# Kernel tuning notes

Hardware: AMD Instinct MI355X
Metric: run time of the kernel (lower is better)

Reference implementation:

```python
import jax, jax.numpy as jnp
import numpy as np

H = 32      # num_attention_heads
HD = 64     # head_dim
MD = 64     # qk_mqa_dim (rope dim)
EPS = 1e-6
SCALING = (HD + MD) ** -0.5
NEG = -1e9


def rms_norm(x, w):
    var = jnp.mean(jnp.square(x), axis=-1, keepdims=True)
    return x * jax.lax.rsqrt(var + EPS) * w


def rotate_half(x):
    x1, x2 = jnp.split(x, 2, axis=-1)
    return jnp.concatenate([-x2, x1], axis=-1)


def apply_rope(x, cos, sin):
    return x * cos + rotate_half(x) * sin


def setup_inputs() -> dict:
    key = jax.random.key(0)
    ks = jax.random.split(key, 6)
    B, S, D = 1, 2048, 2048
    QR, KVR = 1024, 896
    hidden_states = jax.random.normal(ks[0], (B, S, D), jnp.float32)
    # real rotary tables for the MD-dim rope subspace
    inv_freq = 1.0 / (10000.0 ** (np.arange(0, MD, 2, dtype=np.float32) / MD))
    freqs = np.arange(S, dtype=np.float32)[:, None] * inv_freq[None, :]
    emb = np.concatenate([freqs, freqs], axis=-1)  # [S, MD]
    cos = jnp.asarray(np.cos(emb), jnp.float32)
    sin = jnp.asarray(np.sin(emb), jnp.float32)
    s = 0.02
    Wqa = jax.random.normal(ks[1], (QR, D), jnp.float32) * s
    q_ln_w = jnp.ones((QR,), jnp.float32)
    Wqb = jax.random.normal(ks[2], (H * (HD + MD), QR), jnp.float32) * s
    Wkva = jax.random.normal(ks[3], (KVR + MD, D), jnp.float32) * s
    kv_ln_w = jnp.ones((KVR,), jnp.float32)
    Wkvb = jax.random.normal(ks[4], (2 * H * HD, KVR), jnp.float32) * s
    Wo = jax.random.normal(ks[5], (D, H * HD), jnp.float32) * s
    return {"hidden_states": hidden_states, "cos": cos, "sin": sin,
            "Wqa": Wqa, "q_ln_w": q_ln_w, "Wqb": Wqb,
            "Wkva": Wkva, "kv_ln_w": kv_ln_w, "Wkvb": Wkvb, "Wo": Wo}


def reference(hidden_states, cos, sin, Wqa, q_ln_w, Wqb, Wkva, kv_ln_w, Wkvb, Wo):
    B, S, D = hidden_states.shape
    KVR = kv_ln_w.shape[0]
    # Q: LoRA down -> RMSNorm -> up (weights pre-absorbed with rope split)
    q = rms_norm(hidden_states @ Wqa.T, q_ln_w) @ Wqb.T      # [B,S,H*(HD+MD)]
    q = q.reshape(B, S, H, HD + MD).transpose(0, 2, 1, 3)     # [B,H,S,HD+MD]
    q_nope, q_rope = q[..., :HD], q[..., HD:]
    # KV: shared compressed latent + MQA rope key
    ckv = hidden_states @ Wkva.T                               # [B,S,KVR+MD]
    kv_nope, k_rope = ckv[..., :KVR], ckv[..., KVR:]
    kv_nope = rms_norm(kv_nope, kv_ln_w)
    q_rope = apply_rope(q_rope, cos[None, None], sin[None, None])
    k_rope = apply_rope(k_rope[:, None], cos[None, None], sin[None, None])  # [B,1,S,MD]
    # up-project latent to per-head K_nope and V (interleaved per head)
    kv = (kv_nope @ Wkvb.T).reshape(B, S, H, 2 * HD).transpose(0, 2, 1, 3)  # [B,H,S,2*HD]
    k_nope, value = kv[..., :HD], kv[..., HD:]
    key_states = jnp.concatenate(
        [k_nope, jnp.broadcast_to(k_rope, (B, H, S, MD))], axis=-1)  # repeat_kv of rope part
    query_states = jnp.concatenate([q_nope, q_rope], axis=-1)        # [B,H,S,HD+MD]
    # causal SDPA with scaling = (head_dim + qk_mqa_dim)^-0.5
    scores = jnp.einsum('bhqd,bhkd->bhqk', query_states, key_states) * SCALING
    causal = jnp.tril(jnp.ones((S, S), bool))
    scores = jnp.where(causal[None, None], scores, NEG)
    probs = jax.nn.softmax(scores, axis=-1)
    out = jnp.einsum('bhqk,bhkd->bhqd', probs, value)                # [B,H,S,HD]
    out = out.transpose(0, 2, 1, 3).reshape(B, S, H * HD)
    return out @ Wo.T
```

## Files before the change

kernel.cpp:

```cpp
#include <hip/hip_runtime.h>
#include <stdint.h>

typedef unsigned short u16;
typedef __attribute__((ext_vector_type(4))) float f32x4;
typedef __attribute__((ext_vector_type(4))) unsigned short u16x4;
typedef __attribute__((ext_vector_type(8))) unsigned short u16x8;
typedef __attribute__((ext_vector_type(8))) short s16x8;
typedef __attribute__((ext_vector_type(4))) short s16x4;
typedef __attribute__((ext_vector_type(2))) unsigned int u32x2;

#define DEVI static __device__ __forceinline__

#define VMCNT(n) asm volatile("s_waitcnt vmcnt(" #n ")" ::: "memory")
#define SBAR() __builtin_amdgcn_s_barrier()
#define SCHED0() __builtin_amdgcn_sched_barrier(0)

DEVI u16 f2b(float f) {
  union { float f; unsigned u; } v; v.f = f;
  unsigned r = v.u + 0x7fffu + ((v.u >> 16) & 1u);
  return (u16)(r >> 16);
}
DEVI float b2f(u16 b) {
  union { unsigned u; float f; } v; v.u = ((unsigned)b) << 16;
  return v.f;
}

DEVI void gload_lds16(const void* gptr, void* lptr) {
  typedef const __attribute__((address_space(1))) unsigned gq;
  typedef __attribute__((address_space(3))) unsigned lq;
  __builtin_amdgcn_global_load_lds((gq*)(uintptr_t)gptr,
                                   (lq*)(uint32_t)(uintptr_t)lptr, 16, 0, 0);
}

DEVI unsigned cvtpk(float a, float b) {
  unsigned d;
  asm("v_cvt_pk_bf16_f32 %0, %1, %2" : "=v"(d) : "v"(a), "v"(b));
  return d;
}
DEVI f32x4 mfma16(s16x4 a, s16x4 b, f32x4 c) {
  f32x4 d;
  asm("v_mfma_f32_16x16x16_bf16 %0, %1, %2, %3" : "=v"(d) : "v"(a), "v"(b), "v"(c));
  return d;
}
DEVI float exp2a(float x) {
  float d;
  asm("v_exp_f32 %0, %1" : "=v"(d) : "v"(x));
  return d;
}

__global__ __launch_bounds__(256) void cvt_all(
    const float* __restrict__ X, const float* __restrict__ Wqa,
    const float* __restrict__ Wkva, const float* __restrict__ Wqb,
    const float* __restrict__ Wkvb, const float* __restrict__ Wo,
    u16* __restrict__ Xb, u16* __restrict__ W1, u16* __restrict__ Wqbb,
    u16* __restrict__ Wkvbb, u16* __restrict__ Wob) {
  int i = blockIdx.x * 256 + threadIdx.x;
  const int stride = gridDim.x * 256;
  for (; i < 5079040; i += stride) {
    const float* s; u16* d; int j;
    if (i < 1572864) {
      if (i < 1048576) { s = X; d = Xb; j = i; }
      else             { s = Wqa; d = W1; j = i - 1048576; }
    } else if (i < 3112960) {
      if (i < 2064384) { s = Wkva; d = W1 + 1024 * 2048; j = i - 1572864; }
      else             { s = Wqb; d = Wqbb; j = i - 2064384; }
    } else {
      if (i < 4030464) { s = Wkvb; d = Wkvbb; j = i - 3112960; }
      else             { s = Wo; d = Wob; j = i - 4030464; }
    }
    f32x4 v = *(const f32x4*)(s + (size_t)j * 4);
    u16x4 o;
    o[0] = f2b(v[0]); o[1] = f2b(v[1]); o[2] = f2b(v[2]); o[3] = f2b(v[3]);
    *(u16x4*)(d + (size_t)j * 4) = o;
  }
}

#define GEMM_STAGE(AP, BP, KK, k0, buf)                                        \
  {                                                                            \
    _Pragma("unroll") for (int p = 0; p < 4; ++p) {                            \
      const int c = tid + p * 256;                                             \
      const int row = c >> 3, j = c & 7;                                       \
      gload_lds16(AP + (size_t)(m0 + row) * (KK) + (k0) + ((j ^ (row & 7)) * 8), \
                  &As[buf][c * 8]);                                            \
    }                                                                          \
    _Pragma("unroll") for (int p = 0; p < 4; ++p) {                            \
      const int c = tid + p * 256;                                             \
      const int row = c >> 3, j = c & 7;                                       \
      gload_lds16(BP + (size_t)(n0 + row) * (KK) + (k0) + ((j ^ (row & 7)) * 8), \
                  &Bs[buf][c * 8]);                                            \
    }                                                                          \
  }

#define GEMM_COMPUTE(cur)                                                      \
  _Pragma("unroll") for (int kk = 0; kk < 64; kk += 32) {                      \
    s16x8 af[4], bfr[4];                                                       \
    _Pragma("unroll") for (int i = 0; i < 4; ++i) {                            \
      const int rA = wm * 64 + i * 16 + c15;                                   \
      af[i] = *(const s16x8*)((const char*)&As[cur][0] + rA * 128 +            \
                              (((kk + g * 8) * 2) ^ ((rA & 7) << 4)));         \
    }                                                                          \
    _Pragma("unroll") for (int i = 0; i < 4; ++i) {                            \
      const int rB = wn * 64 + i * 16 + c15;                                   \
      bfr[i] = *(const s16x8*)((const char*)&Bs[cur][0] + rB * 128 +           \
                               (((kk + g * 8) * 2) ^ ((rB & 7) << 4)));        \
    }                                                                          \
    _Pragma("unroll") for (int i = 0; i < 4; ++i)                              \
      _Pragma("unroll") for (int j = 0; j < 4; ++j)                            \
        acc[i][j] = __builtin_amdgcn_mfma_f32_16x16x32_bf16(af[i], bfr[j],     \
                                                            acc[i][j], 0, 0, 0); \
  }

#define GEMM_PROLOG                                                            \
  const int tid = threadIdx.x;                                                 \
  const int lane = tid & 63, w = tid >> 6;                                     \
  const int wm = w >> 1, wn = w & 1;                                           \
  const int c15 = lane & 15, g = lane >> 4;                                    \
  const int m0 = blockIdx.y * 128, n0 = blockIdx.x * 128;                      \
  f32x4 acc[4][4] = {};

#define GEMM_LOOP(AP, BP, KK)                                                  \
  GEMM_STAGE(AP, BP, KK, 0, 0);                                                \
  const int nk = (KK) >> 6;                                                    \
  for (int kt = 0; kt < nk; ++kt) {                                            \
    const int cur = kt & 1;                                                    \
    if (kt + 1 < nk) {                                                         \
      GEMM_STAGE(AP, BP, KK, (kt + 1) << 6, cur ^ 1);                          \
      VMCNT(8);                                                                \
    } else {                                                                   \
      VMCNT(0);                                                                \
    }                                                                          \
    SBAR(); SCHED0();                                                          \
    GEMM_COMPUTE(cur);                                                         \
    SBAR(); SCHED0();                                                          \
  }

#define GEMM_LOOP3(AP, BP, KK)                                                 \
  GEMM_STAGE(AP, BP, KK, 0, 0);                                                \
  GEMM_STAGE(AP, BP, KK, 64, 1);                                               \
  const int nk = (KK) >> 6;                                                    \
  int bufc = 0;                                                                \
  for (int kt = 0; kt < nk; ++kt) {                                            \
    const int nxt = (bufc + 2 >= 3) ? bufc - 1 : bufc + 2;                     \
    if (kt + 2 < nk) {                                                         \
      GEMM_STAGE(AP, BP, KK, (kt + 2) << 6, nxt);                              \
      VMCNT(16);                                                               \
    } else if (kt + 1 < nk) {                                                  \
      VMCNT(8);                                                                \
    } else {                                                                   \
      VMCNT(0);                                                                \
    }                                                                          \
    SBAR(); SCHED0();                                                          \
    GEMM_COMPUTE(bufc);                                                        \
    SBAR(); SCHED0();                                                          \
    bufc = (bufc + 1 == 3) ? 0 : bufc + 1;                                     \
  }

template <int OUT_BF16>
__global__ __launch_bounds__(256) void gemm_out(const u16* __restrict__ A,
                                                const u16* __restrict__ B,
                                                void* __restrict__ Cv,
                                                int M, int N, int K) {
  __shared__ __align__(16) u16 As[3][128 * 64];
  __shared__ __align__(16) u16 Bs[3][128 * 64];
  GEMM_PROLOG
  GEMM_LOOP3(A, B, K)
#pragma unroll
  for (int i = 0; i < 4; ++i)
#pragma unroll
    for (int j = 0; j < 4; ++j) {
      const int mr = m0 + wm * 64 + i * 16 + g * 4;
      const int nc = n0 + wn * 64 + j * 16 + c15;
#pragma unroll
      for (int r = 0; r < 4; ++r) {
        if (OUT_BF16)
          ((u16*)Cv)[(size_t)(mr + r) * N + nc] = f2b(acc[i][j][r]);
        else
          ((float*)Cv)[(size_t)(mr + r) * N + nc] = acc[i][j][r];
      }
    }
}

__global__ __launch_bounds__(256) void gemm2_fused(
    const u16* __restrict__ qn, const u16* __restrict__ Wqbb,
    const u16* __restrict__ kvn, const u16* __restrict__ Wkvbb,
    u16* __restrict__ qraw, char* __restrict__ KbB, char* __restrict__ VtB) {
  __shared__ __align__(16) u16 As[2][128 * 64];
  __shared__ __align__(16) u16 Bs[2][128 * 64];
  const int z = blockIdx.z;
  const u16* A = z ? kvn : qn;
  const u16* B = z ? Wkvbb : Wqbb;
  const int K = z ? 896 : 1024;
  GEMM_PROLOG
  GEMM_LOOP(A, B, K)

  if (z == 0) {
#pragma unroll
    for (int i = 0; i < 4; ++i)
#pragma unroll
      for (int j = 0; j < 4; ++j) {
        const int mr = m0 + wm * 64 + i * 16 + g * 4;
        const int nc = n0 + wn * 64 + j * 16 + c15;
#pragma unroll
        for (int r = 0; r < 4; ++r)
          qraw[(size_t)(mr + r) * 4096 + nc] = f2b(acc[i][j][r]);
      }
  } else {
    const int h = n0 >> 7;
#pragma unroll
    for (int i = 0; i < 4; ++i)
#pragma unroll
      for (int j = 0; j < 4; ++j) {
        const int mr = m0 + wm * 64 + i * 16 + g * 4;
        if (wn == 0) {
          const int d = j * 16 + c15;
#pragma unroll
          for (int r = 0; r < 4; ++r) {
            const int s = mr + r;
            *(u16*)(KbB + ((size_t)(h * 2048 + s) << 8) +
                    ((2 * d) ^ ((s & 7) << 4))) = f2b(acc[i][j][r]);
          }
        } else {
          const int d = j * 16 + c15;
          u16x4 o;
#pragma unroll
          for (int r = 0; r < 4; ++r) o[r] = f2b(acc[i][j][r]);
          *(u16x4*)(VtB + ((size_t)(h * 64 + d) << 12) +
                    ((2 * mr) ^ ((d & 7) << 4))) = o;
        }
      }
  }
}

DEVI float block_sum(float v, float* sbuf, int tid) {
#pragma unroll
  for (int o = 32; o; o >>= 1) v += __shfl_xor(v, o, 64);
  __syncthreads();
  if ((tid & 63) == 0) sbuf[tid >> 6] = v;
  __syncthreads();
  return sbuf[0] + sbuf[1] + sbuf[2] + sbuf[3];
}

__global__ __launch_bounds__(256) void norm_rope(const u16* __restrict__ C1b,
    const float* __restrict__ qw, const float* __restrict__ kw,
    const float* __restrict__ cosb, const float* __restrict__ sinb,
    u16* __restrict__ qn, u16* __restrict__ kvn, char* __restrict__ KbB) {
  __shared__ float sbuf[4];
  __shared__ __align__(16) u16 rv[64];
  const int s = blockIdx.x, tid = threadIdx.x;
  const u16* row = C1b + (size_t)s * 2048;

  u16x4 qv4 = *(const u16x4*)(row + tid * 4);
  float q0 = b2f(qv4[0]), q1 = b2f(qv4[1]), q2 = b2f(qv4[2]), q3 = b2f(qv4[3]);
  float ss = q0*q0 + q1*q1 + q2*q2 + q3*q3;
  ss = block_sum(ss, sbuf, tid);
  const float scale = rsqrtf(ss * (1.f / 1024.f) + 1e-6f);
  {
    f32x4 wv = *(const f32x4*)(qw + tid * 4);
    u16x4 o;
    o[0] = f2b(q0 * scale * wv[0]); o[1] = f2b(q1 * scale * wv[1]);
    o[2] = f2b(q2 * scale * wv[2]); o[3] = f2b(q3 * scale * wv[3]);
    *(u16x4*)(qn + (size_t)s * 1024 + tid * 4) = o;
  }

  float ss2 = 0.f;
  float k0 = 0, k1 = 0, k2 = 0, k3 = 0;
  if (tid < 224) {
    u16x4 kv4 = *(const u16x4*)(row + 1024 + tid * 4);
    k0 = b2f(kv4[0]); k1 = b2f(kv4[1]); k2 = b2f(kv4[2]); k3 = b2f(kv4[3]);
    ss2 = k0*k0 + k1*k1 + k2*k2 + k3*k3;
  }
  ss2 = block_sum(ss2, sbuf, tid);
  const float sc2 = rsqrtf(ss2 * (1.f / 896.f) + 1e-6f);
  if (tid < 224) {
    f32x4 wv = *(const f32x4*)(kw + tid * 4);
    u16x4 o;
    o[0] = f2b(k0 * sc2 * wv[0]); o[1] = f2b(k1 * sc2 * wv[1]);
    o[2] = f2b(k2 * sc2 * wv[2]); o[3] = f2b(k3 * sc2 * wv[3]);
    *(u16x4*)(kvn + (size_t)s * 896 + tid * 4) = o;
  }

  if (tid < 64) {
    const int d = tid;
    const float x = b2f(row[1920 + d]);
    const float part = b2f(row[1920 + (d < 32 ? d + 32 : d - 32)]);
    const float cv = cosb[s * 64 + d], sv = sinb[s * 64 + d];
    rv[d] = f2b(d < 32 ? (x * cv - part * sv) : (x * cv + part * sv));
  }
  __syncthreads();
  {
    const int h = tid >> 3, c8 = tid & 7;
    const u16x8 v = *(const u16x8*)&rv[c8 * 8];
    *(u16x8*)(KbB + ((size_t)(h * 2048 + s) << 8) +
              ((128 + c8 * 16) ^ ((s & 7) << 4))) = v;
  }
}

__global__ __launch_bounds__(256) void attn_fwd(
    const u16* __restrict__ Qb, const u16* __restrict__ Kb,
    const u16* __restrict__ Vt, const float* __restrict__ cosb,
    const float* __restrict__ sinb, u16* __restrict__ attn) {
  __shared__ __align__(16) u16 Klds[2][64 * 128];
  __shared__ __align__(16) u16 Vlds[2][64 * 64];
  const int tid = threadIdx.x;
  const int lane = tid & 63, w = tid >> 6;
  const int c15 = lane & 15, g = lane >> 4;
  const int orig = blockIdx.x;
  const int xcd = orig & 7, l = orig >> 3;
  const int h = xcd * 4 + (l & 3);
  const int x = l >> 2;
  const int qb = (x < 8) ? (15 - x) : (x - 8);
  const int wmin = qb * 128 + w * 32;
  const int wmax = wmin + 31;
  const char* KbHB = (const char*)Kb + ((size_t)h << 19);
  const char* VtHB = (const char*)Vt + ((size_t)h << 18);
  const float SC2 = 0.12753860478587782f;

  s16x8 qf[2][4];
#pragma unroll
  for (int qa = 0; qa < 2; ++qa) {
    const int qrow = wmin + qa * 16 + c15;
    const u16* qp = Qb + (size_t)qrow * 4096 + h * 128;
    u16x8 x0 = *(const u16x8*)(qp + g * 8);
    u16x8 x1 = *(const u16x8*)(qp + 32 + g * 8);
    u16x8 x2 = *(const u16x8*)(qp + 64 + g * 8);
    u16x8 x3 = *(const u16x8*)(qp + 96 + g * 8);
    const float* cb = cosb + (size_t)qrow * 64 + g * 8;
    const float* sb = sinb + (size_t)qrow * 64 + g * 8;
#pragma unroll
    for (int i = 0; i < 8; ++i) {
      qf[qa][0][i] = (short)f2b(b2f(x0[i]) * SC2);
      qf[qa][1][i] = (short)f2b(b2f(x1[i]) * SC2);
      const float f2 = b2f(x2[i]), f3 = b2f(x3[i]);
      qf[qa][2][i] = (short)f2b((f2 * cb[i] - f3 * sb[i]) * SC2);
      qf[qa][3][i] = (short)f2b((f3 * cb[32 + i] + f2 * sb[32 + i]) * SC2);
    }
  }

  const int nt = 2 * qb + 2;
  auto STAGE = [&](int t, int buf) {
    const int kv0 = t << 6;
#pragma unroll
    for (int p = 0; p < 4; ++p) {
      const int c = tid + p * 256;
      gload_lds16(KbHB + ((size_t)(kv0 + (c >> 4)) << 8) + (c & 15) * 16,
                  (char*)Klds[buf] + c * 16);
    }
#pragma unroll
    for (int p = 0; p < 2; ++p) {
      const int c = tid + p * 256;
      gload_lds16(VtHB + ((size_t)(c >> 3) << 12) + 2 * kv0 + (c & 7) * 16,
                  (char*)Vlds[buf] + c * 16);
    }
  };

  f32x4 acc[2][4] = {};
  float m[2] = {-1e9f, -1e9f}, ssum[2] = {0.f, 0.f};

  STAGE(0, 0);

  for (int t = 0; t < nt; ++t) {
    const int cur = t & 1;
    const int kv0 = t << 6;
    if (t + 1 < nt) {
      STAGE(t + 1, cur ^ 1);
      VMCNT(6);
    } else {
      VMCNT(0);
    }
    SBAR();
    SCHED0();

    if (kv0 <= wmax) {
      const u16* Kc = Klds[cur];
      const u16* Vc = Vlds[cur];

      float pv[2][4][4];
      __builtin_amdgcn_s_setprio(1);
#pragma unroll
      for (int kvh = 0; kvh < 4; ++kvh) {
        s16x8 kf[4];
        const int rb = (kvh * 16 + c15) * 256;
#pragma unroll
        for (int d0 = 0; d0 < 4; ++d0)
          kf[d0] = *(const s16x8*)((const char*)Kc + rb +
                                   ((d0 * 64 + g * 16) ^ ((c15 & 7) << 4)));
#pragma unroll
        for (int qa = 0; qa < 2; ++qa) {
          f32x4 s4 = {};
#pragma unroll
          for (int d0 = 0; d0 < 4; ++d0)
            s4 = __builtin_amdgcn_mfma_f32_16x16x32_bf16(kf[d0], qf[qa][d0], s4, 0, 0, 0);
          pv[qa][kvh][0] = s4[0]; pv[qa][kvh][1] = s4[1];
          pv[qa][kvh][2] = s4[2]; pv[qa][kvh][3] = s4[3];
        }
      }
      __builtin_amdgcn_s_setprio(0);

      if (kv0 + 63 > wmin) {
#pragma unroll
        for (int qa = 0; qa < 2; ++qa) {
          const int qrow = wmin + qa * 16 + c15;
#pragma unroll
          for (int kvh = 0; kvh < 4; ++kvh)
#pragma unroll
            for (int r = 0; r < 4; ++r) {
              const int kv = kv0 + kvh * 16 + g * 4 + r;
              if (kv > qrow) pv[qa][kvh][r] = -1e9f;
            }
        }
      }

      s16x4 pB[2][4];
#pragma unroll
      for (int qa = 0; qa < 2; ++qa) {
        float pm = -1e9f;
#pragma unroll
        for (int kvh = 0; kvh < 4; ++kvh)
#pragma unroll
          for (int r = 0; r < 4; ++r) pm = fmaxf(pm, pv[qa][kvh][r]);
        pm = fmaxf(pm, __shfl_xor(pm, 16, 64));
        pm = fmaxf(pm, __shfl_xor(pm, 32, 64));
        if (!__all(pm - m[qa] <= 8.f)) {
          const float mnew = fmaxf(m[qa], pm);
          const float alpha = exp2a(m[qa] - mnew);
          ssum[qa] *= alpha;
#pragma unroll
          for (int dt = 0; dt < 4; ++dt) acc[qa][dt] *= alpha;
          m[qa] = mnew;
        }
#pragma unroll
        for (int kvh = 0; kvh < 4; ++kvh)
#pragma unroll
          for (int r = 0; r < 4; ++r) {
            const float p = exp2a(pv[qa][kvh][r] - m[qa]);
            pv[qa][kvh][r] = p;
            ssum[qa] += p;
          }
#pragma unroll
        for (int ks = 0; ks < 4; ++ks) {
          u32x2 pw;
          pw[0] = cvtpk(pv[qa][ks][0], pv[qa][ks][1]);
          pw[1] = cvtpk(pv[qa][ks][2], pv[qa][ks][3]);
          pB[qa][ks] = __builtin_bit_cast(s16x4, pw);
        }
      }

      __builtin_amdgcn_s_setprio(1);
#pragma unroll
      for (int dt = 0; dt < 4; ++dt) {
        const int rb2 = (dt * 16 + c15) * 128;
#pragma unroll
        for (int ks = 0; ks < 4; ++ks) {
          s16x4 vf = *(const s16x4*)((const char*)Vc + rb2 +
                                     ((ks * 32 + g * 8) ^ ((c15 & 7) << 4)));
          acc[0][dt] = mfma16(vf, pB[0][ks], acc[0][dt]);
          acc[1][dt] = mfma16(vf, pB[1][ks], acc[1][dt]);
        }
      }
      __builtin_amdgcn_s_setprio(0);
    }
    SBAR();
    SCHED0();
  }

#pragma unroll
  for (int qa = 0; qa < 2; ++qa) {
    float sv = ssum[qa];
    sv += __shfl_xor(sv, 16, 64);
    sv += __shfl_xor(sv, 32, 64);
    const float inv = 1.f / sv;
    const int qrow = wmin + qa * 16 + c15;
#pragma unroll
    for (int dt = 0; dt < 4; ++dt) {
      u16x4 o;
#pragma unroll
      for (int r = 0; r < 4; ++r) o[r] = f2b(acc[qa][dt][r] * inv);
      *(u16x4*)(attn + (size_t)qrow * 2048 + h * 64 + dt * 16 + g * 4) = o;
    }
  }
}

extern "C" void kernel_launch(void* const* d_in, const int* in_sizes, int n_in,
                              void* d_out, int out_size, void* d_ws, size_t ws_size,
                              hipStream_t stream) {
  const float* X    = (const float*)d_in[0];
  const float* cosb = (const float*)d_in[1];
  const float* sinb = (const float*)d_in[2];
  const float* Wqa  = (const float*)d_in[3];
  const float* qlnw = (const float*)d_in[4];
  const float* Wqb  = (const float*)d_in[5];
  const float* Wkva = (const float*)d_in[6];
  const float* klnw = (const float*)d_in[7];
  const float* Wkvb = (const float*)d_in[8];
  const float* Wo   = (const float*)d_in[9];
  float* out = (float*)d_out;
  char* ws = (char*)d_ws;

  u16*   Xb     = (u16*)(ws + 0);
  u16*   W1     = (u16*)(ws + 8388608);
  u16*   C1b    = (u16*)(ws + 16777216);
  u16*   qn     = (u16*)(ws + 33554432);
  u16*   kvn    = (u16*)(ws + 37748736);
  u16*   Wqbb   = (u16*)(ws + 41943040);
  u16*   Wkvbb  = (u16*)(ws + 50331648);
  u16*   qraw_b = (u16*)(ws + 0);
  u16*   Kb     = (u16*)(ws + 58720256);
  u16*   VtG    = (u16*)(ws + 75497472);
  u16*   attnb  = (u16*)(ws + 83886080);
  u16*   Wob    = (u16*)(ws + 92274688);

  cvt_all<<<2048, 256, 0, stream>>>(X, Wqa, Wkva, Wqb, Wkvb, Wo,
                                    Xb, W1, Wqbb, Wkvbb, Wob);

  gemm_out<1><<<dim3(16, 16), 256, 0, stream>>>(Xb, W1, C1b, 2048, 2048, 2048);

  norm_rope<<<2048, 256, 0, stream>>>(C1b, qlnw, klnw, cosb, sinb, qn, kvn, (char*)Kb);

  gemm2_fused<<<dim3(32, 16, 2), 256, 0, stream>>>(qn, Wqbb, kvn, Wkvbb,
                                                   qraw_b, (char*)Kb, (char*)VtG);

  attn_fwd<<<512, 256, 0, stream>>>(qraw_b, Kb, VtG, cosb, sinb, attnb);

  gemm_out<0><<<dim3(16, 16), 256, 0, stream>>>(attnb, Wob, out, 2048, 2048, 2048);
}
```

Measured before the change: 172.8 us.

## Load V fragments directly from global memory instead of staging through LDS

The attention kernel stops staging V tiles into shared memory. Each wave now reads its V MFMA fragments straight from global memory into registers, using an unswizzled Vt layout written by the producer kernel. The vmcnt wait count is adjusted to match the removed LDS loads. Separately, the cross-lane max reduction in the online softmax is now performed only when a rescale is needed. The aim is to cut LDS traffic and footprint, in exchange for extra global or L2 loads issued by every wave and more register pressure.

```diff
diff --git a/kernel.cpp b/kernel.cpp
--- a/kernel.cpp
+++ b/kernel.cpp
@@ -224,8 +224,7 @@
           u16x4 o;
 #pragma unroll
           for (int r = 0; r < 4; ++r) o[r] = f2b(acc[i][j][r]);
-          *(u16x4*)(VtB + ((size_t)(h * 64 + d) << 12) +
-                    ((2 * mr) ^ ((d & 7) << 4))) = o;
+          *(u16x4*)(VtB + ((size_t)(h * 64 + d) << 12) + 2 * mr) = o;
         }
       }
   }
@@ -298,9 +297,8 @@
 __global__ __launch_bounds__(256) void attn_fwd(
     const u16* __restrict__ Qb, const u16* __restrict__ Kb,
     const u16* __restrict__ Vt, const float* __restrict__ cosb,
-    const float* __restrict__ sinb, u16* __restrict__ attn) {
+    const float* __restrict__ sinb, u16* __restrict__ attnb) {
   __shared__ __align__(16) u16 Klds[2][64 * 128];
-  __shared__ __align__(16) u16 Vlds[2][64 * 64];
   const int tid = threadIdx.x;
   const int lane = tid & 63, w = tid >> 6;
   const int c15 = lane & 15, g = lane >> 4;
@@ -345,12 +343,6 @@
       gload_lds16(KbHB + ((size_t)(kv0 + (c >> 4)) << 8) + (c & 15) * 16,
                   (char*)Klds[buf] + c * 16);
     }
-#pragma unroll
-    for (int p = 0; p < 2; ++p) {
-      const int c = tid + p * 256;
-      gload_lds16(VtHB + ((size_t)(c >> 3) << 12) + 2 * kv0 + (c & 7) * 16,
-                  (char*)Vlds[buf] + c * 16);
-    }
   };
 
   f32x4 acc[2][4] = {};
@@ -363,7 +355,7 @@
     const int kv0 = t << 6;
     if (t + 1 < nt) {
       STAGE(t + 1, cur ^ 1);
-      VMCNT(6);
+      VMCNT(4);
     } else {
       VMCNT(0);
     }
@@ -372,7 +364,15 @@
 
     if (kv0 <= wmax) {
       const u16* Kc = Klds[cur];
-      const u16* Vc = Vlds[cur];
+
+      s16x4 vf[4][4];
+#pragma unroll
+      for (int dt = 0; dt < 4; ++dt) {
+        const char* vp = VtHB + (size_t)(dt * 16 + c15) * 4096 + 2 * (kv0 + g * 4);
+#pragma unroll
+        for (int ks = 0; ks < 4; ++ks)
+          vf[dt][ks] = *(const s16x4*)(vp + ks * 32);
+      }
 
       float pv[2][4][4];
       __builtin_amdgcn_s_setprio(1);
@@ -413,14 +413,14 @@
       s16x4 pB[2][4];
 #pragma unroll
       for (int qa = 0; qa < 2; ++qa) {
-        float pm = -1e9f;
+        float pml = -1e9f;
 #pragma unroll
         for (int kvh = 0; kvh < 4; ++kvh)
 #pragma unroll
-          for (int r = 0; r < 4; ++r) pm = fmaxf(pm, pv[qa][kvh][r]);
-        pm = fmaxf(pm, __shfl_xor(pm, 16, 64));
-        pm = fmaxf(pm, __shfl_xor(pm, 32, 64));
-        if (!__all(pm - m[qa] <= 8.f)) {
+          for (int r = 0; r < 4; ++r) pml = fmaxf(pml, pv[qa][kvh][r]);
+        if (!__all(pml - m[qa] <= 8.f)) {
+          float pm = fmaxf(pml, __shfl_xor(pml, 16, 64));
+          pm = fmaxf(pm, __shfl_xor(pm, 32, 64));
           const float mnew = fmaxf(m[qa], pm);
           const float alpha = exp2a(m[qa] - mnew);
           ssum[qa] *= alpha;
@@ -448,13 +448,10 @@
       __builtin_amdgcn_s_setprio(1);
 #pragma unroll
       for (int dt = 0; dt < 4; ++dt) {
-        const int rb2 = (dt * 16 + c15) * 128;
 #pragma unroll
         for (int ks = 0; ks < 4; ++ks) {
-          s16x4 vf = *(const s16x4*)((const char*)Vc + rb2 +
-                                     ((ks * 32 + g * 8) ^ ((c15 & 7) << 4)));
-          acc[0][dt] = mfma16(vf, pB[0][ks], acc[0][dt]);
-          acc[1][dt] = mfma16(vf, pB[1][ks], acc[1][dt]);
+          acc[0][dt] = mfma16(vf[dt][ks], pB[0][ks], acc[0][dt]);
+          acc[1][dt] = mfma16(vf[dt][ks], pB[1][ks], acc[1][dt]);
         }
       }
       __builtin_amdgcn_s_setprio(0);
@@ -475,7 +472,7 @@
       u16x4 o;
 #pragma unroll
       for (int r = 0; r < 4; ++r) o[r] = f2b(acc[qa][dt][r] * inv);
-      *(u16x4*)(attn + (size_t)qrow * 2048 + h * 64 + dt * 16 + g * 4) = o;
+      *(u16x4*)(attnb + (size_t)qrow * 2048 + h * 64 + dt * 16 + g * 4) = o;
     }
   }
 }
```

New measurement: 202.1 us. +16.9%, slower.
